# Kernel tuning notes

Measured on AMD Instinct MI355X. Metric: run time of the kernel, lower is better.

The kernel has to match this reference:

```python
import jax, jax.numpy as jnp
import numpy as np

WINDOW = 3
FILTER = 6
FEATURE = 768
SEQ = 256
PAD = WINDOW // 2


def setup_inputs() -> dict:
    key = jax.random.key(0)
    k1, k2, k3 = jax.random.split(key, 3)
    B = 256
    inputs = jax.random.normal(k1, (B, SEQ, FEATURE), dtype=jnp.float32)
    # per-position Linear weights: torch nn.Linear stores [out, in]; we keep [S, in, out]
    bound = 1.0 / np.sqrt(WINDOW * FEATURE)
    W = jax.random.uniform(k2, (SEQ, WINDOW * FEATURE, FILTER), dtype=jnp.float32,
                           minval=-bound, maxval=bound)
    b = jax.random.uniform(k3, (SEQ, FILTER), dtype=jnp.float32,
                           minval=-bound, maxval=bound)
    return {"inputs": inputs, "W": W, "b": b}


def reference(inputs, W, b):
    # inputs: [B, S, F]. Pad along sequence with zeros (matches F.pad on transposed tensor).
    padded = jnp.pad(inputs, ((0, 0), (PAD, PAD), (0, 0)))  # [B, S+2p, F]
    # Vectorized sliding-window gather: idx [S, W]
    idx = jnp.arange(SEQ)[:, None] + jnp.arange(WINDOW)[None, :]
    windows = padded[:, idx, :]                              # [B, S, W, F]
    Bsz = windows.shape[0]
    windows = windows.reshape(Bsz, SEQ, WINDOW * FEATURE)    # [B, S, W*F]
    # Per-position distinct Linear + ReLU (Dropout is identity at inference)
    out = jnp.einsum('bsf,sfo->bso', windows, W) + b[None, :, :]
    return jax.nn.relu(out)
```

## Files before the change

### kernel.cpp

```cpp
#include <hip/hip_runtime.h>

#define SEQ   256
#define FEAT  768
#define FILT  6
#define WELEMS (2304 * FILT)

typedef _Float16 f16x8 __attribute__((ext_vector_type(8)));
typedef __attribute__((ext_vector_type(4))) float f32x4;

__global__ __launch_bounds__(512, 4)
void pos_linear_kernel(const float* __restrict__ x,
                       const float* __restrict__ W,
                       const float* __restrict__ bias,
                       float* __restrict__ out) {
    __shared__ __align__(16) unsigned short wf[13824];

    const int blk   = blockIdx.x;
    const int halfb = blk >> 8;
    const int sb    = blk & 255;
    const int s     = ((sb & 7) << 5) | (sb >> 3);
    const int tid   = threadIdx.x;

    {
        const float* Ws = W + (size_t)s * WELEMS;
        for (int k = tid; k < 2304; k += 512) {
            const int slot8 = (k >> 3) * 6;
            const int e     = k & 7;
            #pragma unroll
            for (int o = 0; o < FILT; ++o) {
                _Float16 hv = (_Float16)Ws[k * FILT + o];
                wf[(slot8 + o) * 8 + e] = *(const unsigned short*)&hv;
            }
        }
    }
    __syncthreads();

    const int lane = tid & 63;
    const int wave = tid >> 6;
    const int row  = lane & 15;
    const int h    = lane >> 4;
    const int col  = lane & 15;
    const bool cv  = col < FILT;
    const int b0   = (halfb << 7) + (wave << 4);

    const int bidx = (6 * h + (cv ? col : 5)) * 8;

    f32x4 acc_h = {0, 0, 0, 0};
    f32x4 acc_l = {0, 0, 0, 0};

    const float* xb = x + (size_t)(b0 + row) * (SEQ * FEAT) + 8 * h;

    auto step = [&](f32x4 u, f32x4 v, int tg) {
        f16x8 ah, al;
        #pragma unroll
        for (int e = 0; e < 8; ++e) {
            float f = (e < 4) ? u[e] : v[e - 4];
            _Float16 hh = (_Float16)f;
            ah[e] = hh;
            al[e] = (_Float16)(f - (float)hh);
        }
        f16x8 bw = *(const f16x8*)&wf[bidx + 192 * tg];
        acc_h = __builtin_amdgcn_mfma_f32_16x16x32_f16(ah, bw, acc_h, 0, 0, 0);
        acc_l = __builtin_amdgcn_mfma_f32_16x16x32_f16(al, bw, acc_l, 0, 0, 0);
    };

    #pragma unroll
    for (int p = 0; p < 3; ++p) {
        const int w = (p - s + 256) % 3;
        const int r = s - 1 + w;
        if (r >= 0 && r < SEQ) {
            const f32x4* ap = (const f32x4*)(xb + (size_t)r * FEAT);
            const int tb = 24 * w;

            f32x4 qa[6], qb[6];
            #pragma unroll
            for (int t = 0; t < 6; ++t) { qa[t] = ap[8 * t]; qb[t] = ap[8 * t + 1]; }
            #pragma unroll
            for (int t = 0; t < 24; ++t) {
                f32x4 u = qa[t % 6], v = qb[t % 6];
                if (t + 6 < 24) {
                    qa[t % 6] = ap[8 * (t + 6)];
                    qb[t % 6] = ap[8 * (t + 6) + 1];
                }
                step(u, v, tb + t);
            }
        }
        __syncthreads();
    }

    if (cv) {
        const float bv = bias[s * FILT + col];
        #pragma unroll
        for (int g = 0; g < 4; ++g) {
            const int b = b0 + 4 * h + g;
            float vsum = acc_h[g] + acc_l[g] + bv;
            vsum = vsum > 0.f ? vsum : 0.f;
            out[((size_t)b * SEQ + s) * FILT + col] = vsum;
        }
    }
}

extern "C" void kernel_launch(void* const* d_in, const int* in_sizes, int n_in,
                              void* d_out, int out_size, void* d_ws, size_t ws_size,
                              hipStream_t stream) {
    const float* x   = (const float*)d_in[0];
    const float* W   = (const float*)d_in[1];
    const float* b   = (const float*)d_in[2];
    float*       out = (float*)d_out;
    (void)in_sizes; (void)n_in; (void)out_size; (void)d_ws; (void)ws_size;
    pos_linear_kernel<<<SEQ * 2, 512, 0, stream>>>(x, W, b, out);
}
```

Measured before the change: 298.9 us.

## Process four sequence positions per block to reuse overlapping window rows

```diff
diff --git a/kernel.cpp b/kernel.cpp
--- a/kernel.cpp
+++ b/kernel.cpp
@@ -1,35 +1,45 @@
 #include <hip/hip_runtime.h>
 
-#define SEQ   256
-#define FEAT  768
-#define FILT  6
+#define SEQ    256
+#define FEAT   768
+#define FILT   6
 #define WELEMS (2304 * FILT)
+
+#define QS     4
+#define NROW   6
+#define TPK    6
+#define DEPTH  6
 
 typedef _Float16 f16x8 __attribute__((ext_vector_type(8)));
 typedef __attribute__((ext_vector_type(4))) float f32x4;
 
-__global__ __launch_bounds__(512, 4)
+__global__ __launch_bounds__(1024, 4)
 void pos_linear_kernel(const float* __restrict__ x,
                        const float* __restrict__ W,
                        const float* __restrict__ bias,
                        float* __restrict__ out) {
-    __shared__ __align__(16) unsigned short wf[13824];
+    __shared__ __align__(16) unsigned short wf[QS * 13824];
+    __shared__ float red[2][4096];
 
-    const int blk   = blockIdx.x;
-    const int halfb = blk >> 8;
-    const int sb    = blk & 255;
-    const int s     = ((sb & 7) << 5) | (sb >> 3);
-    const int tid   = threadIdx.x;
+    const int blk  = blockIdx.x;
+    const int xcd  = blk & 7;
+    const int idx  = blk >> 3;
+    const int quad = 8 * xcd + (idx & 7);
+    const int bq   = idx >> 3;
+    const int s0   = 4 * quad;
+    const int tid  = threadIdx.x;
 
-    {
-        const float* Ws = W + (size_t)s * WELEMS;
-        for (int k = tid; k < 2304; k += 512) {
+    #pragma unroll
+    for (int sv = 0; sv < QS; ++sv) {
+        const float* Ws = W + (size_t)(s0 + sv) * WELEMS;
+        unsigned short* wt = wf + sv * 13824;
+        for (int k = tid; k < 2304; k += 1024) {
             const int slot8 = (k >> 3) * 6;
             const int e     = k & 7;
             #pragma unroll
             for (int o = 0; o < FILT; ++o) {
                 _Float16 hv = (_Float16)Ws[k * FILT + o];
-                wf[(slot8 + o) * 8 + e] = *(const unsigned short*)&hv;
+                wt[(slot8 + o) * 8 + e] = *(const unsigned short*)&hv;
             }
         }
     }
@@ -37,20 +47,50 @@
 
     const int lane = tid & 63;
     const int wave = tid >> 6;
-    const int row  = lane & 15;
+    const int mt   = wave >> 2;
+    const int kv   = wave & 3;
+    const int rowm = lane & 15;
     const int h    = lane >> 4;
     const int col  = lane & 15;
     const bool cv  = col < FILT;
-    const int b0   = (halfb << 7) + (wave << 4);
+    const int b0   = bq * 64 + mt * 16;
 
-    const int bidx = (6 * h + (cv ? col : 5)) * 8;
+    const int bidx = (6 * h + (cv ? col : 5)) * 8 + 1152 * kv;
 
-    f32x4 acc_h = {0, 0, 0, 0};
-    f32x4 acc_l = {0, 0, 0, 0};
+    f32x4 acc_h[QS], acc_l[QS];
+    #pragma unroll
+    for (int sv = 0; sv < QS; ++sv) {
+        acc_h[sv] = (f32x4){0.f, 0.f, 0.f, 0.f};
+        acc_l[sv] = (f32x4){0.f, 0.f, 0.f, 0.f};
+    }
 
-    const float* xb = x + (size_t)(b0 + row) * (SEQ * FEAT) + 8 * h;
+    const float* xb = x + (size_t)(b0 + rowm) * (SEQ * FEAT) + 8 * h + 192 * kv;
+    const f32x4* rp[NROW];
+    bool rv[NROW];
+    #pragma unroll
+    for (int q = 0; q < NROW; ++q) {
+        const int r = s0 - 1 + q;
+        rv[q] = (r >= 0) && (r < SEQ);
+        rp[q] = (const f32x4*)(xb + (size_t)(rv[q] ? r : 0) * FEAT);
+    }
 
-    auto step = [&](f32x4 u, f32x4 v, int tg) {
+    f32x4 qa[DEPTH], qb[DEPTH];
+    #pragma unroll
+    for (int g = 0; g < DEPTH; ++g) {
+        qa[g] = rp[0][8 * g];
+        qb[g] = rp[0][8 * g + 1];
+    }
+
+    #pragma unroll
+    for (int g = 0; g < NROW * TPK; ++g) {
+        const int rho  = g / TPK;
+        const int tloc = g % TPK;
+        f32x4 u = qa[g % DEPTH], v = qb[g % DEPTH];
+        if (g + DEPTH < NROW * TPK) {
+            const int gn = g + DEPTH;
+            qa[g % DEPTH] = rp[gn / TPK][8 * (gn % TPK)];
+            qb[g % DEPTH] = rp[gn / TPK][8 * (gn % TPK) + 1];
+        }
         f16x8 ah, al;
         #pragma unroll
         for (int e = 0; e < 8; ++e) {
@@ -59,43 +99,67 @@
             ah[e] = hh;
             al[e] = (_Float16)(f - (float)hh);
         }
-        f16x8 bw = *(const f16x8*)&wf[bidx + 192 * tg];
-        acc_h = __builtin_amdgcn_mfma_f32_16x16x32_f16(ah, bw, acc_h, 0, 0, 0);
-        acc_l = __builtin_amdgcn_mfma_f32_16x16x32_f16(al, bw, acc_l, 0, 0, 0);
-    };
-
-    #pragma unroll
-    for (int p = 0; p < 3; ++p) {
-        const int w = (p - s + 256) % 3;
-        const int r = s - 1 + w;
-        if (r >= 0 && r < SEQ) {
-            const f32x4* ap = (const f32x4*)(xb + (size_t)r * FEAT);
-            const int tb = 24 * w;
-
-            f32x4 qa[6], qb[6];
+        if (rv[rho]) {
             #pragma unroll
-            for (int t = 0; t < 6; ++t) { qa[t] = ap[8 * t]; qb[t] = ap[8 * t + 1]; }
-            #pragma unroll
-            for (int t = 0; t < 24; ++t) {
-                f32x4 u = qa[t % 6], v = qb[t % 6];
-                if (t + 6 < 24) {
-                    qa[t % 6] = ap[8 * (t + 6)];
-                    qb[t % 6] = ap[8 * (t + 6) + 1];
-                }
-                step(u, v, tb + t);
+            for (int sv = 0; sv < QS; ++sv) {
+                const int w = rho - sv;
+                if (w < 0 || w > 2) continue;
+                const f16x8 bw = *(const f16x8*)
+                    &wf[bidx + sv * 13824 + 4608 * w + 192 * tloc];
+                acc_h[sv] = __builtin_amdgcn_mfma_f32_16x16x32_f16(
+                                ah, bw, acc_h[sv], 0, 0, 0);
+                acc_l[sv] = __builtin_amdgcn_mfma_f32_16x16x32_f16(
+                                al, bw, acc_l[sv], 0, 0, 0);
             }
         }
-        __syncthreads();
+        if (tloc == TPK - 1) __syncthreads();
     }
 
-    if (cv) {
-        const float bv = bias[s * FILT + col];
+    float tot[QS][4];
+    #pragma unroll
+    for (int sv = 0; sv < QS; ++sv)
         #pragma unroll
-        for (int g = 0; g < 4; ++g) {
-            const int b = b0 + 4 * h + g;
-            float vsum = acc_h[g] + acc_l[g] + bv;
-            vsum = vsum > 0.f ? vsum : 0.f;
-            out[((size_t)b * SEQ + s) * FILT + col] = vsum;
+        for (int gg = 0; gg < 4; ++gg)
+            tot[sv][gg] = acc_h[sv][gg] + acc_l[sv][gg];
+
+    if (kv == 1 || kv == 3) {
+        float* rb = red[kv >> 1];
+        #pragma unroll
+        for (int sv = 0; sv < QS; ++sv)
+            #pragma unroll
+            for (int gg = 0; gg < 4; ++gg)
+                rb[((mt * QS + sv) * 4 + gg) * 64 + lane] = tot[sv][gg];
+    }
+    __syncthreads();
+    if (kv == 0 || kv == 2) {
+        const float* rb = red[kv >> 1];
+        #pragma unroll
+        for (int sv = 0; sv < QS; ++sv)
+            #pragma unroll
+            for (int gg = 0; gg < 4; ++gg)
+                tot[sv][gg] += rb[((mt * QS + sv) * 4 + gg) * 64 + lane];
+    }
+    __syncthreads();
+    if (kv == 2) {
+        #pragma unroll
+        for (int sv = 0; sv < QS; ++sv)
+            #pragma unroll
+            for (int gg = 0; gg < 4; ++gg)
+                red[0][((mt * QS + sv) * 4 + gg) * 64 + lane] = tot[sv][gg];
+    }
+    __syncthreads();
+    if (kv == 0 && cv) {
+        #pragma unroll
+        for (int sv = 0; sv < QS; ++sv) {
+            const float bv = bias[(s0 + sv) * FILT + col];
+            #pragma unroll
+            for (int gg = 0; gg < 4; ++gg) {
+                const int b = b0 + 4 * h + gg;
+                float val = tot[sv][gg] +
+                            red[0][((mt * QS + sv) * 4 + gg) * 64 + lane] + bv;
+                val = val > 0.f ? val : 0.f;
+                out[((size_t)b * SEQ + (s0 + sv)) * FILT + col] = val;
+            }
         }
     }
 }
@@ -108,5 +172,5 @@
     const float* b   = (const float*)d_in[2];
     float*       out = (float*)d_out;
     (void)in_sizes; (void)n_in; (void)out_size; (void)d_ws; (void)ws_size;
-    pos_linear_kernel<<<SEQ * 2, 512, 0, stream>>>(x, W, b, out);
+    pos_linear_kernel<<<256, 1024, 0, stream>>>(x, W, b, out);
 }
```

Measured after the change: 306.9 us. 1.03x slower.
